# Performance work log

Measured on AMD Instinct MI355X. Metric: run time of the kernel, lower is better.

## Reference

```python
import jax, jax.numpy as jnp
import numpy as np

H = 1024          # hidden_size
M = 512           # moe_intermediate_size
E = 16            # num_routed_experts
TOP_K = 2         # num_experts_per_tok
SCALE = 2.5       # routed_scaling_factor
NORM_TOPK = True  # norm_topk_prob
B, S = 1, 1024


def setup_inputs() -> dict:
    key = jax.random.key(0)
    ks = jax.random.split(key, 8)
    std = 0.02
    return {
        "hidden_states": jax.random.normal(ks[0], (B, S, H), jnp.float32),
        "gate_w": jax.random.normal(ks[1], (E, H), jnp.float32) * std,
        "w_gate": jax.random.normal(ks[2], (E, H, M), jnp.float32) * std,
        "w_up": jax.random.normal(ks[3], (E, H, M), jnp.float32) * std,
        "w_down": jax.random.normal(ks[4], (E, M, H), jnp.float32) * std,
        "ws_gate": jax.random.normal(ks[5], (H, M), jnp.float32) * std,
        "ws_up": jax.random.normal(ks[6], (H, M), jnp.float32) * std,
        "ws_down": jax.random.normal(ks[7], (M, H), jnp.float32) * std,
    }


def _moe(x, gate_w, w_gate, w_up, w_down, ws_gate, ws_up, ws_down):
    # x: [T, H] flattened tokens
    T = x.shape[0]
    # shared expert (SwiGLU): down(silu(gate(x)) * up(x))
    shared = (jax.nn.silu(x @ ws_gate) * (x @ ws_up)) @ ws_down  # [T, H]

    # sigmoid gating in fp32 (matches F.linear on fp32 + sigmoid)
    scores = jax.nn.sigmoid(x.astype(jnp.float32) @ gate_w.T.astype(jnp.float32))  # [T, E]
    topk_w, topk_idx = jax.lax.top_k(scores, TOP_K)  # [T, K]
    if NORM_TOPK and TOP_K > 1:
        topk_w = topk_w / (topk_w.sum(-1, keepdims=True) + 1e-20)
    topk_w = topk_w * SCALE

    # dense combine weights [T, E]; zero for non-selected experts, so weighting
    # all-expert outputs is mathematically identical to the dispatch/gather path
    route = jnp.zeros((T, E), topk_w.dtype).at[jnp.arange(T)[:, None], topk_idx].set(topk_w)

    # per-expert SwiGLU over all tokens (grouped-GEMM reference)
    g = jnp.einsum("th,ehm->etm", x, w_gate)                 # [E, T, M]
    u = jnp.einsum("th,ehm->etm", x, w_up)                   # [E, T, M]
    eo = jnp.einsum("etm,emh->eth", jax.nn.silu(g) * u, w_down)  # [E, T, H]
    routed = jnp.einsum("te,eth->th", route.astype(x.dtype), eo)  # [T, H]
    return routed + shared


def reference(hidden_states, gate_w, w_gate, w_up, w_down, ws_gate, ws_up, ws_down):
    b, s, h = hidden_states.shape
    x = hidden_states.reshape(-1, h)
    out = _moe(x, gate_w, w_gate, w_up, w_down, ws_gate, ws_up, ws_down)
    return out.reshape(b, s, h)
```

## Files before the change

### kernel.cpp

```cpp
#include <hip/hip_runtime.h>
#include <math.h>

#define TT 1024
#define HH 1024
#define MM 512
#define NE 16

typedef _Float16 f16;
typedef _Float16 f16x8 __attribute__((ext_vector_type(8)));
typedef float f32x4 __attribute__((ext_vector_type(4)));

#define GLL(g, l) __builtin_amdgcn_global_load_lds(                         \
    (const __attribute__((address_space(1))) void*)(g),                     \
    (__attribute__((address_space(3))) void*)(l), 16, 0, 0)

#define SB() __builtin_amdgcn_sched_barrier(0)
#define WAITVM(N) { SB(); asm volatile("s_waitcnt vmcnt(" #N ")"); SB(); }
#define BARRIER() __builtin_amdgcn_s_barrier()

__global__ __launch_bounds__(256) void router_k(
    const float* __restrict__ x, const float* __restrict__ gate_w,
    int* __restrict__ counts, int* __restrict__ token_list, float* __restrict__ weight_list)
{
    const int wave = threadIdx.x >> 6;
    const int lane = threadIdx.x & 63;
    const int t = (blockIdx.x << 2) + wave;
    const float* xr = x + (size_t)t * HH;
    float xv[16];
#pragma unroll
    for (int i = 0; i < 16; ++i) xv[i] = xr[lane + (i << 6)];
    float sc[NE];
#pragma unroll
    for (int e = 0; e < NE; ++e) {
        const float* gr = gate_w + e * HH;
        float acc = 0.f;
#pragma unroll
        for (int i = 0; i < 16; ++i) acc = fmaf(xv[i], gr[lane + (i << 6)], acc);
#pragma unroll
        for (int off = 32; off > 0; off >>= 1) acc += __shfl_down(acc, off, 64);
        sc[e] = acc;
    }
    if (lane == 0) {
        float l1 = -1e30f, l2 = -1e30f; int i1 = 0, i2 = 0;
#pragma unroll
        for (int e = 0; e < NE; ++e) {
            float v = sc[e];
            if (v > l1) { l2 = l1; i2 = i1; l1 = v; i1 = e; }
            else if (v > l2) { l2 = v; i2 = e; }
        }
        float w1 = 1.f / (1.f + __expf(-l1));
        float w2 = 1.f / (1.f + __expf(-l2));
        const float inv = 2.5f / (w1 + w2 + 1e-20f);
        w1 *= inv; w2 *= inv;
        int s1 = atomicAdd(&counts[i1], 1);
        token_list[i1 * TT + s1] = t;
        weight_list[i1 * TT + s1] = w1;
        int s2 = atomicAdd(&counts[i2], 1);
        token_list[i2 * TT + s2] = t;
        weight_list[i2 * TT + s2] = w2;
    }
}

__global__ void prefix_k(const int* __restrict__ counts, int* __restrict__ offs)
{
    if (threadIdx.x == 0 && blockIdx.x == 0) {
        int acc = 0;
#pragma unroll
        for (int e = 0; e < NE; ++e) { offs[e] = acc; acc += counts[e]; }
        offs[NE] = acc;
    }
}


#define GU_ISSUE(K0, AS, BG, BU) {                                          \
    _Pragma("unroll") for (int i = 0; i < 4; ++i)                           \
        GLL(pA[i] + (K0), &AS[aw + 4*i][0]);                                \
    _Pragma("unroll") for (int i = 0; i < 2; ++i) {                         \
        GLL(pBg[i] + (size_t)(K0) * MM, &BG[(w << 4) + 8*i][0]);            \
        GLL(pBu[i] + (size_t)(K0) * MM, &BU[(w << 4) + 8*i][0]); } }

#define GU_COMP(AS, BG, BU) {                                               \
    _Pragma("unroll") for (int h = 0; h < 2; ++h) {                         \
        const int kb = (h << 5) + (lg << 3);                                \
        const int xr = (lm & 7) << 2;                                       \
        f16x8 af[2];                                                        \
        _Pragma("unroll") for (int f = 0; f < 2; ++f) {                     \
            const int m = wm + (f << 4) + lm;                               \
            float4 lo = *(const float4*)&AS[m][kb ^ xr];                    \
            float4 hi = *(const float4*)&AS[m][(kb + 4) ^ xr];              \
            af[f] = (f16x8){(f16)lo.x,(f16)lo.y,(f16)lo.z,(f16)lo.w,        \
                            (f16)hi.x,(f16)hi.y,(f16)hi.z,(f16)hi.w};       \
        }                                                                   \
        const int bc = (wn + lm) ^ ((lg & 1) << 4);                         \
        f16x8 bg, bu;                                                       \
        _Pragma("unroll") for (int j = 0; j < 8; ++j) {                     \
            bg[j] = (f16)BG[kb + j][bc]; bu[j] = (f16)BU[kb + j][bc]; }     \
        _Pragma("unroll") for (int f = 0; f < 2; ++f) {                     \
            accg[f] = __builtin_amdgcn_mfma_f32_16x16x32_f16(af[f], bg, accg[f], 0, 0, 0); \
            accu[f] = __builtin_amdgcn_mfma_f32_16x16x32_f16(af[f], bu, accu[f], 0, 0, 0); } } }

__global__ __launch_bounds__(256) void gu_k(
    const float* __restrict__ x,
    const float* __restrict__ w_gate, const float* __restrict__ w_up,
    const float* __restrict__ ws_gate, const float* __restrict__ ws_up,
    const int* __restrict__ counts, const int* __restrict__ offs,
    const int* __restrict__ token_list, f16* __restrict__ rinter)
{
    const int e = blockIdx.z;
    int cnt, slot0;
    const float *wgp, *wup;
    if (e < NE) {
        cnt = counts[e]; slot0 = offs[e];
        wgp = w_gate + (size_t)e * HH * MM;
        wup = w_up   + (size_t)e * HH * MM;
    } else {
        cnt = TT; slot0 = 2 * TT;
        wgp = ws_gate; wup = ws_up;
    }
    const int r0 = blockIdx.y << 6;
    if (r0 >= cnt) return;
    const int n0 = blockIdx.x << 5;

    __shared__ float As0[64][64], As1[64][64];
    __shared__ float Bg0[64][32], Bg1[64][32];
    __shared__ float Bu0[64][32], Bu1[64][32];
    __shared__ int toks[64];

    const int tid = threadIdx.x;
    if (tid < 64) {
        int i = r0 + tid; if (i >= cnt) i = cnt - 1;
        toks[tid] = (e < NE) ? token_list[e * TT + i] : i;
    }
    __syncthreads();

    const int w = tid >> 6, lane = tid & 63;
    const int lm = lane & 15, lg = lane >> 4;
    const int wm = (w >> 1) << 5, wn = (w & 1) << 4;
    const int aw = w << 4;

    const float* pA[4];
#pragma unroll
    for (int i = 0; i < 4; ++i) {
        int m = aw + 4*i + (lane >> 4);
        pA[i] = x + (size_t)toks[m] * HH + 4 * ((lane & 15) ^ (m & 7));
    }
    const float* pBg[2]; const float* pBu[2];
#pragma unroll
    for (int i = 0; i < 2; ++i) {
        int kr = (w << 4) + 8*i + (lane >> 3);
        int sg = 4 * ((lane & 7) ^ ((i & 1) << 2));
        pBg[i] = wgp + (size_t)kr * MM + n0 + sg;
        pBu[i] = wup + (size_t)kr * MM + n0 + sg;
    }

    f32x4 accg[2] = {}, accu[2] = {};

    GU_ISSUE(0, As0, Bg0, Bu0)
#pragma unroll 1
    for (int t = 0; t < 14; t += 2) {
        GU_ISSUE((t + 1) << 6, As1, Bg1, Bu1)
        WAITVM(8) BARRIER();
        GU_COMP(As0, Bg0, Bu0)
        BARRIER();
        GU_ISSUE((t + 2) << 6, As0, Bg0, Bu0)
        WAITVM(8) BARRIER();
        GU_COMP(As1, Bg1, Bu1)
        BARRIER();
    }
    GU_ISSUE(15 << 6, As1, Bg1, Bu1)
    WAITVM(8) BARRIER();
    GU_COMP(As0, Bg0, Bu0)
    BARRIER();
    WAITVM(0) BARRIER();
    GU_COMP(As1, Bg1, Bu1)

#pragma unroll
    for (int fi = 0; fi < 2; ++fi)
#pragma unroll
        for (int rr = 0; rr < 4; ++rr) {
            const int m = wm + (fi << 4) + (lg << 2) + rr;
            if (r0 + m < cnt) {
                float g = accg[fi][rr], u = accu[fi][rr];
                float s = g / (1.f + __expf(-g));
                rinter[(size_t)(slot0 + r0 + m) * MM + n0 + wn + lm] = (f16)(s * u);
            }
        }
}


#define DN_ISSUE(K0, AS, BS) {                                              \
    _Pragma("unroll") for (int i = 0; i < 2; ++i) {                         \
        GLL(pa[i] + (K0), &AS[(w << 4) + 8*i][0]);                          \
        GLL(pb[i] + (size_t)(K0) * HH, &BS[(w << 4) + 8*i][0]); } }

#define DN_COMP(AS, BS) {                                                   \
    _Pragma("unroll") for (int h = 0; h < 2; ++h) {                         \
        const int kb = (h << 5) + (lg << 3);                                \
        const int xr = (lm & 7) << 3;                                       \
        f16x8 af[2];                                                        \
        _Pragma("unroll") for (int f = 0; f < 2; ++f)                       \
            af[f] = *(const f16x8*)&AS[wm + (f << 4) + lm][kb ^ xr];        \
        const int bc = (wn + lm) ^ ((lg & 1) << 4);                         \
        f16x8 bv;                                                           \
        _Pragma("unroll") for (int j = 0; j < 8; ++j) bv[j] = (f16)BS[kb + j][bc]; \
        _Pragma("unroll") for (int f = 0; f < 2; ++f)                       \
            acc[f] = __builtin_amdgcn_mfma_f32_16x16x32_f16(af[f], bv, acc[f], 0, 0, 0); } }

__global__ __launch_bounds__(256) void down_k(
    const f16* __restrict__ rinter,
    const float* __restrict__ w_down, const float* __restrict__ ws_down,
    const int* __restrict__ counts, const int* __restrict__ offs,
    const int* __restrict__ token_list, const float* __restrict__ weight_list,
    float* __restrict__ out)
{
    const int e = blockIdx.z;
    int cnt, slot0; const float* wdp;
    if (e < NE) { cnt = counts[e]; slot0 = offs[e]; wdp = w_down + (size_t)e * MM * HH; }
    else        { cnt = TT; slot0 = 2 * TT; wdp = ws_down; }
    const int r0 = blockIdx.y << 6;
    if (r0 >= cnt) return;
    const int n0 = blockIdx.x << 5;

    __shared__ f16  As0[64][64], As1[64][64];
    __shared__ float Bs0[64][32], Bs1[64][32];

    const int tid = threadIdx.x;
    const int w = tid >> 6, lane = tid & 63;
    const int lm = lane & 15, lg = lane >> 4;
    const int wm = (w >> 1) << 5, wn = (w & 1) << 4;

    const f16* pa[2]; const float* pb[2];
#pragma unroll
    for (int i = 0; i < 2; ++i) {
        int m = (w << 4) + 8*i + (lane >> 3);
        pa[i] = rinter + (size_t)(slot0 + r0 + m) * MM + 8 * ((lane & 7) ^ (m & 7));
        int kr = (w << 4) + 8*i + (lane >> 3);
        pb[i] = wdp + (size_t)kr * HH + n0 + 4 * ((lane & 7) ^ ((i & 1) << 2));
    }

    f32x4 acc[2] = {};

    DN_ISSUE(0, As0, Bs0)
#pragma unroll 1
    for (int t = 0; t < 6; t += 2) {
        DN_ISSUE((t + 1) << 6, As1, Bs1)
        WAITVM(4) BARRIER();
        DN_COMP(As0, Bs0)
        BARRIER();
        DN_ISSUE((t + 2) << 6, As0, Bs0)
        WAITVM(4) BARRIER();
        DN_COMP(As1, Bs1)
        BARRIER();
    }
    DN_ISSUE(7 << 6, As1, Bs1)
    WAITVM(4) BARRIER();
    DN_COMP(As0, Bs0)
    BARRIER();
    WAITVM(0) BARRIER();
    DN_COMP(As1, Bs1)

#pragma unroll
    for (int fi = 0; fi < 2; ++fi)
#pragma unroll
        for (int rr = 0; rr < 4; ++rr) {
            const int m = wm + (fi << 4) + (lg << 2) + rr;
            const int row = r0 + m;
            if (row < cnt) {
                int t; float wt;
                if (e < NE) { t = token_list[e * TT + row]; wt = weight_list[e * TT + row]; }
                else        { t = row; wt = 1.f; }
                atomicAdd(&out[(size_t)t * HH + n0 + wn + lm], wt * acc[fi][rr]);
            }
        }
}

extern "C" void kernel_launch(void* const* d_in, const int* in_sizes, int n_in,
                              void* d_out, int out_size, void* d_ws, size_t ws_size,
                              hipStream_t stream)
{
    const float* x       = (const float*)d_in[0];
    const float* gate_w  = (const float*)d_in[1];
    const float* w_gate  = (const float*)d_in[2];
    const float* w_up    = (const float*)d_in[3];
    const float* w_down  = (const float*)d_in[4];
    const float* ws_gate = (const float*)d_in[5];
    const float* ws_up   = (const float*)d_in[6];
    const float* ws_down = (const float*)d_in[7];
    float* out = (float*)d_out;

    int* counts = (int*)d_ws;
    int* offs = counts + 16;
    int* token_list = counts + 64;
    float* weight_list = (float*)(counts + 64 + NE * TT);
    f16* rinter = (f16*)(counts + 64 + 2 * NE * TT);

    hipMemsetAsync(counts, 0, 64, stream);
    hipMemsetAsync(out, 0, (size_t)TT * HH * sizeof(float), stream);
    router_k<<<dim3(TT / 4), 256, 0, stream>>>(x, gate_w, counts, token_list, weight_list);
    prefix_k<<<1, 64, 0, stream>>>(counts, offs);
    gu_k<<<dim3(MM / 32, TT / 64, NE + 1), 256, 0, stream>>>(
        x, w_gate, w_up, ws_gate, ws_up, counts, offs, token_list, rinter);
    down_k<<<dim3(HH / 32, TT / 64, NE + 1), 256, 0, stream>>>(
        rinter, w_down, ws_down, counts, offs, token_list, weight_list, out);
}
```

Baseline: 115.2 us.

## Enlarge row tiles to 256, load A directly to registers, triple-buffer weights

Both expert GEMM kernels now give each block up to 256 token rows instead of 64. Each wave owns its own 16-row slices and reads activations straight from global memory into registers, while only the weight tiles are staged through LDS with a three-deep rotation. The aim is to re-read each weight tile fewer times across row-blocks and to drop the LDS traffic for activations. In exchange there are fewer blocks, more accumulator registers, and uncoalesced direct activation loads.

```diff
diff --git a/kernel.cpp b/kernel.cpp
--- a/kernel.cpp
+++ b/kernel.cpp
@@ -13,7 +13,6 @@
 #define GLL(g, l) __builtin_amdgcn_global_load_lds(                         \
     (const __attribute__((address_space(1))) void*)(g),                     \
     (__attribute__((address_space(3))) void*)(l), 16, 0, 0)
-
 #define SB() __builtin_amdgcn_sched_barrier(0)
 #define WAITVM(N) { SB(); asm volatile("s_waitcnt vmcnt(" #N ")"); SB(); }
 #define BARRIER() __builtin_amdgcn_s_barrier()
@@ -72,32 +71,37 @@
 }
 
 
-#define GU_ISSUE(K0, AS, BG, BU) {                                          \
-    _Pragma("unroll") for (int i = 0; i < 4; ++i)                           \
-        GLL(pA[i] + (K0), &AS[aw + 4*i][0]);                                \
-    _Pragma("unroll") for (int i = 0; i < 2; ++i) {                         \
-        GLL(pBg[i] + (size_t)(K0) * MM, &BG[(w << 4) + 8*i][0]);            \
-        GLL(pBu[i] + (size_t)(K0) * MM, &BU[(w << 4) + 8*i][0]); } }
-
-#define GU_COMP(AS, BG, BU) {                                               \
+#define GU_ISSUE(K0, BG, BU) {                                              \
+    _Pragma("unroll") for (int j = 0; j < 2; ++j) {                         \
+        GLL(pbg[j] + (size_t)(K0) * MM, &BG[(w << 4) + (j << 3)][0]);       \
+        GLL(pbu[j] + (size_t)(K0) * MM, &BU[(w << 4) + (j << 3)][0]); } }
+
+#define GU_PH(T, VC, BGc, BUc, BGi, BUi) {                                  \
+    WAITVM(VC)                                                              \
+    BARRIER();                                                              \
+    float4 alo[4][2], ahi[4][2];                                            \
+    _Pragma("unroll") for (int mt = 0; mt < 4; ++mt) if (mact[mt])          \
+      _Pragma("unroll") for (int h = 0; h < 2; ++h) {                       \
+        const float* ap = pa[mt] + ((T) << 6) + (h << 5);                   \
+        alo[mt][h] = *(const float4*)ap; ahi[mt][h] = *(const float4*)(ap + 4); } \
+    SB();                                                                   \
+    if ((T) + 2 < 16) { GU_ISSUE(((T) + 2) << 6, BGi, BUi) }                \
+    SB();                                                                   \
     _Pragma("unroll") for (int h = 0; h < 2; ++h) {                         \
-        const int kb = (h << 5) + (lg << 3);                                \
-        const int xr = (lm & 7) << 2;                                       \
-        f16x8 af[2];                                                        \
-        _Pragma("unroll") for (int f = 0; f < 2; ++f) {                     \
-            const int m = wm + (f << 4) + lm;                               \
-            float4 lo = *(const float4*)&AS[m][kb ^ xr];                    \
-            float4 hi = *(const float4*)&AS[m][(kb + 4) ^ xr];              \
-            af[f] = (f16x8){(f16)lo.x,(f16)lo.y,(f16)lo.z,(f16)lo.w,        \
-                            (f16)hi.x,(f16)hi.y,(f16)hi.z,(f16)hi.w};       \
-        }                                                                   \
-        const int bc = (wn + lm) ^ ((lg & 1) << 4);                         \
-        f16x8 bg, bu;                                                       \
-        _Pragma("unroll") for (int j = 0; j < 8; ++j) {                     \
-            bg[j] = (f16)BG[kb + j][bc]; bu[j] = (f16)BU[kb + j][bc]; }     \
-        _Pragma("unroll") for (int f = 0; f < 2; ++f) {                     \
-            accg[f] = __builtin_amdgcn_mfma_f32_16x16x32_f16(af[f], bg, accg[f], 0, 0, 0); \
-            accu[f] = __builtin_amdgcn_mfma_f32_16x16x32_f16(af[f], bu, accu[f], 0, 0, 0); } } }
+      const int kb = (h << 5) + (lg << 3);                                  \
+      f16x8 bg[2], bu[2];                                                   \
+      _Pragma("unroll") for (int fj = 0; fj < 2; ++fj) {                    \
+        const int bc = ((fj << 4) + lm) ^ ((lg & 1) << 4);                  \
+        _Pragma("unroll") for (int jj = 0; jj < 8; ++jj) {                  \
+          bg[fj][jj] = (f16)BGc[kb + jj][bc];                               \
+          bu[fj][jj] = (f16)BUc[kb + jj][bc]; } }                           \
+      _Pragma("unroll") for (int mt = 0; mt < 4; ++mt) if (mact[mt]) {      \
+        float4 lo = alo[mt][h], hi = ahi[mt][h];                            \
+        f16x8 av = {(f16)lo.x,(f16)lo.y,(f16)lo.z,(f16)lo.w,                \
+                    (f16)hi.x,(f16)hi.y,(f16)hi.z,(f16)hi.w};               \
+        _Pragma("unroll") for (int fj = 0; fj < 2; ++fj) {                  \
+          accg[mt][fj] = __builtin_amdgcn_mfma_f32_16x16x32_f16(av, bg[fj], accg[mt][fj], 0, 0, 0); \
+          accu[mt][fj] = __builtin_amdgcn_mfma_f32_16x16x32_f16(av, bu[fj], accu[mt][fj], 0, 0, 0); } } } }
 
 __global__ __launch_bounds__(256) void gu_k(
     const float* __restrict__ x,
@@ -117,94 +121,96 @@
         cnt = TT; slot0 = 2 * TT;
         wgp = ws_gate; wup = ws_up;
     }
-    const int r0 = blockIdx.y << 6;
-    if (r0 >= cnt) return;
+    const int rbase = blockIdx.y << 8;
+    if (rbase >= cnt) return;
     const int n0 = blockIdx.x << 5;
 
-    __shared__ float As0[64][64], As1[64][64];
-    __shared__ float Bg0[64][32], Bg1[64][32];
-    __shared__ float Bu0[64][32], Bu1[64][32];
-    __shared__ int toks[64];
+    __shared__ float Bg0[64][32], Bu0[64][32];
+    __shared__ float Bg1[64][32], Bu1[64][32];
+    __shared__ float Bg2[64][32], Bu2[64][32];
+    __shared__ int toks[256];
 
     const int tid = threadIdx.x;
-    if (tid < 64) {
-        int i = r0 + tid; if (i >= cnt) i = cnt - 1;
+    {
+        int i = rbase + tid; if (i >= cnt) i = cnt - 1;
         toks[tid] = (e < NE) ? token_list[e * TT + i] : i;
     }
     __syncthreads();
 
     const int w = tid >> 6, lane = tid & 63;
     const int lm = lane & 15, lg = lane >> 4;
-    const int wm = (w >> 1) << 5, wn = (w & 1) << 4;
-    const int aw = w << 4;
-
-    const float* pA[4];
-#pragma unroll
-    for (int i = 0; i < 4; ++i) {
-        int m = aw + 4*i + (lane >> 4);
-        pA[i] = x + (size_t)toks[m] * HH + 4 * ((lane & 15) ^ (m & 7));
-    }
-    const float* pBg[2]; const float* pBu[2];
-#pragma unroll
-    for (int i = 0; i < 2; ++i) {
-        int kr = (w << 4) + 8*i + (lane >> 3);
-        int sg = 4 * ((lane & 7) ^ ((i & 1) << 2));
-        pBg[i] = wgp + (size_t)kr * MM + n0 + sg;
-        pBu[i] = wup + (size_t)kr * MM + n0 + sg;
-    }
-
-    f32x4 accg[2] = {}, accu[2] = {};
-
-    GU_ISSUE(0, As0, Bg0, Bu0)
-#pragma unroll 1
-    for (int t = 0; t < 14; t += 2) {
-        GU_ISSUE((t + 1) << 6, As1, Bg1, Bu1)
-        WAITVM(8) BARRIER();
-        GU_COMP(As0, Bg0, Bu0)
-        BARRIER();
-        GU_ISSUE((t + 2) << 6, As0, Bg0, Bu0)
-        WAITVM(8) BARRIER();
-        GU_COMP(As1, Bg1, Bu1)
-        BARRIER();
-    }
-    GU_ISSUE(15 << 6, As1, Bg1, Bu1)
-    WAITVM(8) BARRIER();
-    GU_COMP(As0, Bg0, Bu0)
-    BARRIER();
-    WAITVM(0) BARRIER();
-    GU_COMP(As1, Bg1, Bu1)
-
-#pragma unroll
-    for (int fi = 0; fi < 2; ++fi)
-#pragma unroll
-        for (int rr = 0; rr < 4; ++rr) {
-            const int m = wm + (fi << 4) + (lg << 2) + rr;
-            if (r0 + m < cnt) {
-                float g = accg[fi][rr], u = accu[fi][rr];
-                float s = g / (1.f + __expf(-g));
-                rinter[(size_t)(slot0 + r0 + m) * MM + n0 + wn + lm] = (f16)(s * u);
+
+    const float* pbg[2]; const float* pbu[2];
+#pragma unroll
+    for (int j = 0; j < 2; ++j) {
+        int r  = (w << 4) + (j << 3) + (lane >> 3);
+        int cs = ((lane & 7) << 2) ^ (((r >> 3) & 1) << 4);
+        pbg[j] = wgp + (size_t)r * MM + n0 + cs;
+        pbu[j] = wup + (size_t)r * MM + n0 + cs;
+    }
+
+    const bool mact[4] = { true, rbase + 64 < cnt, rbase + 128 < cnt, rbase + 192 < cnt };
+    const float* pa[4];
+#pragma unroll
+    for (int mt = 0; mt < 4; ++mt) {
+        int li = (mt << 6) + (w << 4) + lm;
+        pa[mt] = x + (size_t)toks[li] * HH + (lg << 3);
+    }
+
+    f32x4 accg[4][2] = {}, accu[4][2] = {};
+
+    GU_ISSUE(0,  Bg0, Bu0)
+    GU_ISSUE(64, Bg1, Bu1)
+
+    GU_PH(0, 4, Bg0, Bu0, Bg2, Bu2)  GU_PH(1, 4, Bg1, Bu1, Bg0, Bu0)
+    GU_PH(2, 4, Bg2, Bu2, Bg1, Bu1)  GU_PH(3, 4, Bg0, Bu0, Bg2, Bu2)
+    GU_PH(4, 4, Bg1, Bu1, Bg0, Bu0)  GU_PH(5, 4, Bg2, Bu2, Bg1, Bu1)
+    GU_PH(6, 4, Bg0, Bu0, Bg2, Bu2)  GU_PH(7, 4, Bg1, Bu1, Bg0, Bu0)
+    GU_PH(8, 4, Bg2, Bu2, Bg1, Bu1)  GU_PH(9, 4, Bg0, Bu0, Bg2, Bu2)
+    GU_PH(10, 4, Bg1, Bu1, Bg0, Bu0) GU_PH(11, 4, Bg2, Bu2, Bg1, Bu1)
+    GU_PH(12, 4, Bg0, Bu0, Bg2, Bu2) GU_PH(13, 4, Bg1, Bu1, Bg0, Bu0)
+    GU_PH(14, 4, Bg2, Bu2, Bg0, Bu0) GU_PH(15, 0, Bg0, Bu0, Bg0, Bu0)
+
+#pragma unroll
+    for (int mt = 0; mt < 4; ++mt) if (mact[mt])
+#pragma unroll
+        for (int fj = 0; fj < 2; ++fj)
+#pragma unroll
+            for (int rr = 0; rr < 4; ++rr) {
+                int row = rbase + (mt << 6) + (w << 4) + (lg << 2) + rr;
+                if (row < cnt) {
+                    float g = accg[mt][fj][rr], u = accu[mt][fj][rr];
+                    float s = g / (1.f + __expf(-g));
+                    rinter[(size_t)(slot0 + row) * MM + n0 + (fj << 4) + lm] = (f16)(s * u);
+                }
             }
-        }
-}
-
-
-#define DN_ISSUE(K0, AS, BS) {                                              \
-    _Pragma("unroll") for (int i = 0; i < 2; ++i) {                         \
-        GLL(pa[i] + (K0), &AS[(w << 4) + 8*i][0]);                          \
-        GLL(pb[i] + (size_t)(K0) * HH, &BS[(w << 4) + 8*i][0]); } }
-
-#define DN_COMP(AS, BS) {                                                   \
+}
+
+
+#define DN_ISSUE(K0, BD) {                                                  \
+    _Pragma("unroll") for (int j = 0; j < 2; ++j)                           \
+        GLL(pbd[j] + (size_t)(K0) * HH, &BD[(w << 4) + (j << 3)][0]); }
+
+#define DN_PH(T, VC, BDc, BDi) {                                            \
+    WAITVM(VC)                                                              \
+    BARRIER();                                                              \
+    f16x8 av[4][2];                                                         \
+    _Pragma("unroll") for (int mt = 0; mt < 4; ++mt) if (mact[mt])          \
+      _Pragma("unroll") for (int h = 0; h < 2; ++h)                         \
+        av[mt][h] = *(const f16x8*)(pa[mt] + ((T) << 6) + (h << 5));        \
+    SB();                                                                   \
+    if ((T) + 2 < 8) { DN_ISSUE(((T) + 2) << 6, BDi) }                      \
+    SB();                                                                   \
     _Pragma("unroll") for (int h = 0; h < 2; ++h) {                         \
-        const int kb = (h << 5) + (lg << 3);                                \
-        const int xr = (lm & 7) << 3;                                       \
-        f16x8 af[2];                                                        \
-        _Pragma("unroll") for (int f = 0; f < 2; ++f)                       \
-            af[f] = *(const f16x8*)&AS[wm + (f << 4) + lm][kb ^ xr];        \
-        const int bc = (wn + lm) ^ ((lg & 1) << 4);                         \
-        f16x8 bv;                                                           \
-        _Pragma("unroll") for (int j = 0; j < 8; ++j) bv[j] = (f16)BS[kb + j][bc]; \
-        _Pragma("unroll") for (int f = 0; f < 2; ++f)                       \
-            acc[f] = __builtin_amdgcn_mfma_f32_16x16x32_f16(af[f], bv, acc[f], 0, 0, 0); } }
+      const int kb = (h << 5) + (lg << 3);                                  \
+      f16x8 bd[2];                                                          \
+      _Pragma("unroll") for (int fj = 0; fj < 2; ++fj) {                    \
+        const int bc = ((fj << 4) + lm) ^ ((lg & 1) << 4);                  \
+        _Pragma("unroll") for (int jj = 0; jj < 8; ++jj)                    \
+          bd[fj][jj] = (f16)BDc[kb + jj][bc]; }                             \
+      _Pragma("unroll") for (int mt = 0; mt < 4; ++mt) if (mact[mt])        \
+        _Pragma("unroll") for (int fj = 0; fj < 2; ++fj)                    \
+          acc[mt][fj] = __builtin_amdgcn_mfma_f32_16x16x32_f16(av[mt][h], bd[fj], acc[mt][fj], 0, 0, 0); } }
 
 __global__ __launch_bounds__(256) void down_k(
     const f16* __restrict__ rinter,
@@ -217,61 +223,55 @@
     int cnt, slot0; const float* wdp;
     if (e < NE) { cnt = counts[e]; slot0 = offs[e]; wdp = w_down + (size_t)e * MM * HH; }
     else        { cnt = TT; slot0 = 2 * TT; wdp = ws_down; }
-    const int r0 = blockIdx.y << 6;
-    if (r0 >= cnt) return;
+    const int rbase = blockIdx.y << 8;
+    if (rbase >= cnt) return;
     const int n0 = blockIdx.x << 5;
 
-    __shared__ f16  As0[64][64], As1[64][64];
-    __shared__ float Bs0[64][32], Bs1[64][32];
+    __shared__ float Bd0[64][32], Bd1[64][32], Bd2[64][32];
 
     const int tid = threadIdx.x;
     const int w = tid >> 6, lane = tid & 63;
     const int lm = lane & 15, lg = lane >> 4;
-    const int wm = (w >> 1) << 5, wn = (w & 1) << 4;
-
-    const f16* pa[2]; const float* pb[2];
-#pragma unroll
-    for (int i = 0; i < 2; ++i) {
-        int m = (w << 4) + 8*i + (lane >> 3);
-        pa[i] = rinter + (size_t)(slot0 + r0 + m) * MM + 8 * ((lane & 7) ^ (m & 7));
-        int kr = (w << 4) + 8*i + (lane >> 3);
-        pb[i] = wdp + (size_t)kr * HH + n0 + 4 * ((lane & 7) ^ ((i & 1) << 2));
-    }
-
-    f32x4 acc[2] = {};
-
-    DN_ISSUE(0, As0, Bs0)
-#pragma unroll 1
-    for (int t = 0; t < 6; t += 2) {
-        DN_ISSUE((t + 1) << 6, As1, Bs1)
-        WAITVM(4) BARRIER();
-        DN_COMP(As0, Bs0)
-        BARRIER();
-        DN_ISSUE((t + 2) << 6, As0, Bs0)
-        WAITVM(4) BARRIER();
-        DN_COMP(As1, Bs1)
-        BARRIER();
-    }
-    DN_ISSUE(7 << 6, As1, Bs1)
-    WAITVM(4) BARRIER();
-    DN_COMP(As0, Bs0)
-    BARRIER();
-    WAITVM(0) BARRIER();
-    DN_COMP(As1, Bs1)
-
-#pragma unroll
-    for (int fi = 0; fi < 2; ++fi)
-#pragma unroll
-        for (int rr = 0; rr < 4; ++rr) {
-            const int m = wm + (fi << 4) + (lg << 2) + rr;
-            const int row = r0 + m;
-            if (row < cnt) {
-                int t; float wt;
-                if (e < NE) { t = token_list[e * TT + row]; wt = weight_list[e * TT + row]; }
-                else        { t = row; wt = 1.f; }
-                atomicAdd(&out[(size_t)t * HH + n0 + wn + lm], wt * acc[fi][rr]);
+
+    const float* pbd[2];
+#pragma unroll
+    for (int j = 0; j < 2; ++j) {
+        int r  = (w << 4) + (j << 3) + (lane >> 3);
+        int cs = ((lane & 7) << 2) ^ (((r >> 3) & 1) << 4);
+        pbd[j] = wdp + (size_t)r * HH + n0 + cs;
+    }
+
+    const bool mact[4] = { true, rbase + 64 < cnt, rbase + 128 < cnt, rbase + 192 < cnt };
+    const f16* pa[4];
+#pragma unroll
+    for (int mt = 0; mt < 4; ++mt) {
+        int row = rbase + (mt << 6) + (w << 4) + lm;
+        pa[mt] = rinter + (size_t)(slot0 + row) * MM + (lg << 3);
+    }
+
+    f32x4 acc[4][2] = {};
+
+    DN_ISSUE(0,  Bd0)
+    DN_ISSUE(64, Bd1)
+
+    DN_PH(0, 2, Bd0, Bd2) DN_PH(1, 2, Bd1, Bd0) DN_PH(2, 2, Bd2, Bd1)
+    DN_PH(3, 2, Bd0, Bd2) DN_PH(4, 2, Bd1, Bd0) DN_PH(5, 2, Bd2, Bd1)
+    DN_PH(6, 2, Bd0, Bd0) DN_PH(7, 0, Bd1, Bd0)
+
+#pragma unroll
+    for (int mt = 0; mt < 4; ++mt) if (mact[mt])
+#pragma unroll
+        for (int fj = 0; fj < 2; ++fj)
+#pragma unroll
+            for (int rr = 0; rr < 4; ++rr) {
+                int row = rbase + (mt << 6) + (w << 4) + (lg << 2) + rr;
+                if (row < cnt) {
+                    int t; float wt;
+                    if (e < NE) { t = token_list[e * TT + row]; wt = weight_list[e * TT + row]; }
+                    else        { t = row; wt = 1.f; }
+                    atomicAdd(&out[(size_t)t * HH + n0 + (fj << 4) + lm], wt * acc[mt][fj][rr]);
+                }
             }
-        }
 }
 
 extern "C" void kernel_launch(void* const* d_in, const int* in_sizes, int n_in,
@@ -298,8 +298,8 @@
     hipMemsetAsync(out, 0, (size_t)TT * HH * sizeof(float), stream);
     router_k<<<dim3(TT / 4), 256, 0, stream>>>(x, gate_w, counts, token_list, weight_list);
     prefix_k<<<1, 64, 0, stream>>>(counts, offs);
-    gu_k<<<dim3(MM / 32, TT / 64, NE + 1), 256, 0, stream>>>(
+    gu_k<<<dim3(MM / 32, 4, NE + 1), 256, 0, stream>>>(
         x, w_gate, w_up, ws_gate, ws_up, counts, offs, token_list, rinter);
-    down_k<<<dim3(HH / 32, TT / 64, NE + 1), 256, 0, stream>>>(
+    down_k<<<dim3(HH / 32, 4, NE + 1), 256, 0, stream>>>(
         rinter, w_down, ws_down, counts, offs, token_list, weight_list, out);
 }
```

New measurement: 176.5 us. 53.3% more time.
